# Optimization experiments

Hardware: AMD Instinct MI355X
Metric: run time of the kernel (lower is better)

## Reference

```python
import jax, jax.numpy as jnp
import numpy as np

B, S, D, H = 2, 2048, 768, 12
DK = D // H


def setup_inputs() -> dict:
    key = jax.random.key(0)
    ks = jax.random.split(key, 10)
    sc = 0.02
    return {
        "k": jax.random.normal(ks[0], (B, S, D), jnp.float32),
        "q": jax.random.normal(ks[1], (B, S, D), jnp.float32),
        "v": jax.random.normal(ks[2], (B, S, D), jnp.float32),
        "mask": jnp.ones((B, 1, S, S), jnp.int32),
        "wq": jax.random.normal(ks[3], (D, D), jnp.float32) * sc,
        "bq": jnp.zeros((D,), jnp.float32),
        "wk": jax.random.normal(ks[4], (D, D), jnp.float32) * sc,
        "bk": jnp.zeros((D,), jnp.float32),
        "wv": jax.random.normal(ks[5], (D, D), jnp.float32) * sc,
        "bv": jnp.zeros((D,), jnp.float32),
        "wo": jax.random.normal(ks[6], (D, D), jnp.float32) * sc,
        "bo": jnp.zeros((D,), jnp.float32),
    }


def reference(k, q, v, mask, wq, bq, wk, bk, wv, bv, wo, bo):
    # Linear projections (torch Linear: x @ W^T + b)
    query = q @ wq.T + bq
    key_ = k @ wk.T + bk
    value = v @ wv.T + bv
    # [B,S,D] -> [B,H,S,DK]
    def split_heads(x):
        return x.reshape(B, S, H, DK).transpose(0, 2, 1, 3)
    Q, K, V = split_heads(query), split_heads(key_), split_heads(value)
    # NOTE: original masked_fill result is discarded -> mask is a no-op.
    scores = jnp.einsum("bhqd,bhkd->bhqk", Q, K) / jnp.sqrt(jnp.float32(DK))
    attn = jax.nn.softmax(scores, axis=-1)  # dropout p=0.0 -> identity
    out = jnp.einsum("bhqk,bhkd->bhqd", attn, V)
    out = out.transpose(0, 2, 1, 3).reshape(B, S, D)
    return out @ wo.T + bo
```

## Files before the change

### kernel.cpp

```cpp
#include <hip/hip_runtime.h>
#include <hip/hip_bf16.h>

#define B_  2
#define S_  2048
#define D_  768
#define H_  12
#define DK_ 64
#define NX_ (B_*S_*D_)
#define NW_ (D_*D_)
#define CSC 0.18033688011112042f

typedef __attribute__((ext_vector_type(8))) short  bf16x8;
typedef __attribute__((ext_vector_type(4))) float  f32x4;

__device__ __forceinline__ unsigned short f2bf(float f) {
    unsigned int u = __float_as_uint(f);
    u += 0x7fffu + ((u >> 16) & 1u);
    return (unsigned short)(u >> 16);
}

__device__ __forceinline__ unsigned pack_bf2(float a, float b) {
    const unsigned ua = __float_as_uint(a) + 0x8000u;
    const unsigned ub = __float_as_uint(b) + 0x8000u;
    return __builtin_amdgcn_perm(ub, ua, 0x07060302u);
}

__device__ __forceinline__ void async_cp16(const unsigned short* g,
                                           const unsigned short* lds_uniform_base) {
    __builtin_amdgcn_global_load_lds(
        (const __attribute__((address_space(1))) unsigned int*)(uintptr_t)g,
        (__attribute__((address_space(3))) unsigned int*)(unsigned int)(uintptr_t)lds_uniform_base,
        16, 0, 0);
}

struct CvtArgs { const float* s[7]; };

__global__ __launch_bounds__(256) void cvt_all(CvtArgs a,
                                               unsigned short* __restrict__ Xsw,
                                               unsigned short* __restrict__ Wsw) {
    const int bx = blockIdx.x;
    int y, inner;
    if (bx < 2304) { y = bx / 768;             inner = bx % 768; }
    else           { y = 3 + (bx - 2304) / 144; inner = (bx - 2304) % 144; }
    const int idx = inner * 256 + threadIdx.x;
    const int n  = idx / 48;
    const int g2 = idx % 48;
    const float* src = a.s[y] + (long)n * D_ + g2 * 16;
    const float zs = (y == 3) ? CSC : 1.0f;
    unsigned short o[16];
#pragma unroll
    for (int i = 0; i < 4; i++) {
        const float4 f = *(const float4*)(src + i * 4);
        o[i*4+0] = f2bf(f.x*zs); o[i*4+1] = f2bf(f.y*zs);
        o[i*4+2] = f2bf(f.z*zs); o[i*4+3] = f2bf(f.w*zs);
    }
    unsigned short* dst = (y >= 3) ? (Wsw + (long)(y - 3) * NW_ + (long)n * D_)
                                   : (Xsw + (long)y * NX_ + (long)n * D_);
    const int key = n & 7;
#pragma unroll
    for (int h = 0; h < 2; h++) {
        const int g8 = g2 * 2 + h;
        const int kdst = (g8 >> 3) * 64 + (((g8 & 7) ^ key) * 8);
        *(uint4*)(dst + kdst) = *(const uint4*)&o[h * 8];
    }
}

struct QkvArgs { const float* bias[3]; unsigned short* out[3]; };

__global__ __launch_bounds__(256, 3) void gemm_qkv(QkvArgs args,
                                                   const unsigned short* __restrict__ Xsw,
                                                   const unsigned short* __restrict__ Wsw) {
    __shared__ __align__(16) unsigned short smem[17408];
    unsigned short* As = smem;
    unsigned short* Bs = smem + 8192;

    const int t    = threadIdx.x;
    const int wave = t >> 6;
    const int lane = t & 63;
    const int l16  = lane & 15;
    const int quad = lane >> 4;
    const int wm   = wave >> 1, wn = wave & 1;
    const int m0   = blockIdx.x * 128;
    const int zz   = blockIdx.y / 6;
    const int nb   = blockIdx.y % 6;
    const int n0   = nb * 128;

    const unsigned short* Ap = Xsw + (long)zz * NX_;
    const unsigned short* Wp = Wsw + (long)zz * NW_;

    f32x4 acc[4][4];
#pragma unroll
    for (int s = 0; s < 4; s++)
#pragma unroll
        for (int j = 0; j < 4; j++) acc[s][j] = (f32x4){0.f, 0.f, 0.f, 0.f};

    const int lrow = lane >> 3;
    const int lcg  = lane & 7;

    for (int k0 = 0; k0 < D_; k0 += 64) {
        __syncthreads();
#pragma unroll
        for (int i = 0; i < 4; i++) {
            const int chunk = wave * 4 + i;
            async_cp16(Ap + (long)(m0 + chunk * 8 + lrow) * D_ + k0 + lcg * 8,
                       As + chunk * 512);
        }
#pragma unroll
        for (int i = 0; i < 4; i++) {
            const int chunk = wave * 4 + i;
            async_cp16(Wp + (long)(n0 + chunk * 8 + lrow) * D_ + k0 + lcg * 8,
                       Bs + chunk * 512);
        }
        __syncthreads();
#pragma unroll
        for (int ks = 0; ks < 2; ks++) {
            const int cg = ks * 4 + quad;
            bf16x8 af[4], bf[4];
#pragma unroll
            for (int s = 0; s < 4; s++) {
                const int r = wm * 64 + s * 16 + l16;
                af[s] = *(const bf16x8*)&As[r * 64 + ((cg ^ (r & 7)) * 8)];
            }
#pragma unroll
            for (int j = 0; j < 4; j++) {
                const int r = wn * 64 + j * 16 + l16;
                bf[j] = *(const bf16x8*)&Bs[r * 64 + ((cg ^ (r & 7)) * 8)];
            }
#pragma unroll
            for (int s = 0; s < 4; s++)
#pragma unroll
                for (int j = 0; j < 4; j++)
                    acc[s][j] = __builtin_amdgcn_mfma_f32_16x16x32_bf16(af[s], bf[j], acc[s][j], 0, 0, 0);
        }
    }
    __syncthreads();

    const int b     = m0 >> 11;
    const int sbase = m0 & (S_ - 1);
    const float zs  = (zz == 0) ? CSC : 1.0f;
    float bv[4];
#pragma unroll
    for (int j = 0; j < 4; j++) bv[j] = args.bias[zz][n0 + wn * 64 + j * 16 + l16] * zs;

    if (zz < 2) {
        unsigned short* Ls = smem;
#pragma unroll
        for (int s = 0; s < 4; s++)
#pragma unroll
            for (int j = 0; j < 4; j++)
#pragma unroll
                for (int r = 0; r < 4; r++)
                    Ls[(wm * 64 + s * 16 + quad * 4 + r) * 136 + wn * 64 + j * 16 + l16] =
                        f2bf(acc[s][j][r] + bv[j]);
        __syncthreads();
        const int row  = t >> 1;
        const int half = t & 1;
        unsigned short* Op = args.out[zz];
#pragma unroll
        for (int i = 0; i < 8; i++) {
            const int col  = half * 64 + i * 8;
            const int head = nb * 2 + half;
            const uint4 v = *(const uint4*)&Ls[row * 136 + col];
            *(uint4*)(Op + ((long)(b * H_ + head) * S_ + sbase + row) * DK_ + (col & 63)) = v;
        }
    } else {
        unsigned short* Ls = smem;
#pragma unroll
        for (int s = 0; s < 4; s++)
#pragma unroll
            for (int j = 0; j < 4; j++)
#pragma unroll
                for (int r = 0; r < 4; r++) {
                    const int dk  = j * 16 + l16;
                    const int pos = wm * 64 + (quad * 4 + r) * 4 + s;
                    Ls[wn * 8704 + dk * 136 + pos] = f2bf(acc[s][j][r] + bv[j]);
                }
        __syncthreads();
        const int rowIdx = t >> 1;
        const int hh = rowIdx >> 6, dk = rowIdx & 63;
        const int half = t & 1;
        unsigned short* Op = args.out[2];
#pragma unroll
        for (int i = 0; i < 8; i++) {
            const int col = half * 64 + i * 8;
            const uint4 v = *(const uint4*)&Ls[hh * 8704 + dk * 136 + col];
            const int head = nb * 2 + hh;
            *(uint4*)(Op + ((long)(b * H_ + head) * DK_ + dk) * S_ + sbase + col) = v;
        }
    }
}

__global__ __launch_bounds__(256, 3) void attn_kernel(
    const unsigned short* __restrict__ Q, const unsigned short* __restrict__ K,
    const unsigned short* __restrict__ Vt, unsigned short* __restrict__ Ao)
{
    const int t    = threadIdx.x;
    const int wave = t >> 6;
    const int lane = t & 63;
    const int l16  = lane & 15;
    const int quad = lane >> 4;
    const int bid  = blockIdx.x;
    const int bh    = bid % 24;
    const int qtile = bid / 24;

    const unsigned short* Qp = Q  + (long)bh * S_ * DK_;
    const unsigned short* Kp = K  + (long)bh * S_ * DK_;
    const unsigned short* Vp = Vt + (long)bh * DK_ * S_;

    __shared__ __align__(16) unsigned short smem[23040];
    unsigned short* Ps = smem + 18432;

    bf16x8 qfrag[2];
    {
        const long qoff = (long)(qtile * 64 + wave * 16 + l16) * DK_ + quad * 8;
        qfrag[0] = *(const bf16x8*)(Qp + qoff);
        qfrag[1] = *(const bf16x8*)(Qp + qoff + 32);
    }

    const int srow = t >> 2;
    const int scg  = (t & 3) * 16;
    uint4 kreg[2], vreg[2];
    const unsigned short* gk = Kp + (long)srow * DK_ + scg;
    const unsigned short* gv = Vp + (long)srow * S_ + scg;
    kreg[0] = *(const uint4*)gk;  kreg[1] = *(const uint4*)(gk + 8);
    vreg[0] = *(const uint4*)gv;  vreg[1] = *(const uint4*)(gv + 8);
    gk += 64 * DK_;  gv += 64;
    *(uint4*)&smem[srow * 72 + scg]            = kreg[0];
    *(uint4*)&smem[srow * 72 + scg + 8]        = kreg[1];
    *(uint4*)&smem[9216 + srow * 72 + scg]     = vreg[0];
    *(uint4*)&smem[9216 + srow * 72 + scg + 8] = vreg[1];

    f32x4 oacc[4];
#pragma unroll
    for (int j = 0; j < 4; j++) oacc[j] = (f32x4){0.f, 0.f, 0.f, 0.f};
    float lsum[4] = {0.f, 0.f, 0.f, 0.f};

    for (int it = 0; it < 32; ++it) {
        const int co = (it & 1) * 4608;
        const int no = ((it & 1) ^ 1) * 4608;
        __syncthreads();
        const unsigned short* Ks = smem + co;
        const unsigned short* Vs = smem + 9216 + co;

        if (it < 31) {
            kreg[0] = *(const uint4*)gk;  kreg[1] = *(const uint4*)(gk + 8);
            vreg[0] = *(const uint4*)gv;  vreg[1] = *(const uint4*)(gv + 8);
            gk += 64 * DK_;  gv += 64;
        }

        f32x4 sacc[4];
#pragma unroll
        for (int j = 0; j < 4; j++) sacc[j] = (f32x4){0.f, 0.f, 0.f, 0.f};
#pragma unroll
        for (int ks = 0; ks < 2; ks++)
#pragma unroll
            for (int j = 0; j < 4; j++) {
                const bf16x8 bf = *(const bf16x8*)&Ks[(j * 16 + l16) * 72 + ks * 32 + quad * 8];
                sacc[j] = __builtin_amdgcn_mfma_f32_16x16x32_bf16(qfrag[ks], bf, sacc[j], 0, 0, 0);
            }

#pragma unroll
        for (int r = 0; r < 4; r++) {
            const float p0 = exp2f(sacc[0][r]);
            const float p1 = exp2f(sacc[1][r]);
            const float p2 = exp2f(sacc[2][r]);
            const float p3 = exp2f(sacc[3][r]);
            lsum[r] += (p0 + p1) + (p2 + p3);
            uint2 pk = {pack_bf2(p0, p1), pack_bf2(p2, p3)};
            *(uint2*)&Ps[(wave * 16 + quad * 4 + r) * 72 + l16 * 4] = pk;
        }

#pragma unroll
        for (int ks = 0; ks < 2; ks++) {
            const bf16x8 pf = *(const bf16x8*)&Ps[(wave * 16 + l16) * 72 + ks * 32 + quad * 8];
#pragma unroll
            for (int j = 0; j < 4; j++) {
                const bf16x8 vf = *(const bf16x8*)&Vs[(j * 16 + l16) * 72 + ks * 32 + quad * 8];
                oacc[j] = __builtin_amdgcn_mfma_f32_16x16x32_bf16(pf, vf, oacc[j], 0, 0, 0);
            }
        }

        if (it < 31) {
            *(uint4*)&smem[no + srow * 72 + scg]            = kreg[0];
            *(uint4*)&smem[no + srow * 72 + scg + 8]        = kreg[1];
            *(uint4*)&smem[9216 + no + srow * 72 + scg]     = vreg[0];
            *(uint4*)&smem[9216 + no + srow * 72 + scg + 8] = vreg[1];
        }
    }

#pragma unroll
    for (int r = 0; r < 4; r++) {
#pragma unroll
        for (int off = 1; off < 16; off <<= 1)
            lsum[r] += __shfl_xor(lsum[r], off, 64);
        lsum[r] = 1.f / lsum[r];
    }

    __syncthreads();
#pragma unroll
    for (int j = 0; j < 4; j++)
#pragma unroll
        for (int r = 0; r < 4; r++)
            Ps[(wave * 16 + quad * 4 + r) * 72 + j * 16 + l16] =
                f2bf(oacc[j][r] * lsum[r]);

    const int b = bh / H_, h = bh % H_;
    const int row = t >> 2;
    const int c0  = (t & 3) * 16;
    const int qrow = qtile * 64 + row;
    const int key  = qrow & 7;
    const uint4 v0 = *(const uint4*)&Ps[row * 72 + c0];
    const uint4 v1 = *(const uint4*)&Ps[row * 72 + c0 + 8];
    const int g8 = c0 >> 3;
    unsigned short* dst = Ao + (long)(b * S_ + qrow) * D_ + h * DK_;
    *(uint4*)(dst + ((g8 ^ key) * 8))       = v0;
    *(uint4*)(dst + (((g8 + 1) ^ key) * 8)) = v1;
}

__global__ __launch_bounds__(256, 4) void gemm_out(
    const unsigned short* __restrict__ A, const unsigned short* __restrict__ Wsw,
    const float* __restrict__ bias, float* __restrict__ Out)
{
    __shared__ __align__(16) unsigned short smem[8704];
    unsigned short* As = smem;
    unsigned short* Bs = smem + 4096;

    const int t    = threadIdx.x;
    const int wave = t >> 6;
    const int lane = t & 63;
    const int l16  = lane & 15;
    const int quad = lane >> 4;
    const int wm   = wave >> 1, wn = wave & 1;
    const int m0   = blockIdx.x * 64;
    const int n0   = blockIdx.y * 64;

    f32x4 acc[2][2];
#pragma unroll
    for (int s = 0; s < 2; s++)
#pragma unroll
        for (int j = 0; j < 2; j++) acc[s][j] = (f32x4){0.f, 0.f, 0.f, 0.f};

    const int lrow = lane >> 3;
    const int lcg  = lane & 7;

    for (int k0 = 0; k0 < D_; k0 += 64) {
        __syncthreads();
#pragma unroll
        for (int i = 0; i < 2; i++) {
            const int chunk = wave * 2 + i;
            async_cp16(A + (long)(m0 + chunk * 8 + lrow) * D_ + k0 + lcg * 8,
                       As + chunk * 512);
        }
#pragma unroll
        for (int i = 0; i < 2; i++) {
            const int chunk = wave * 2 + i;
            async_cp16(Wsw + (long)(n0 + chunk * 8 + lrow) * D_ + k0 + lcg * 8,
                       Bs + chunk * 512);
        }
        __syncthreads();
#pragma unroll
        for (int ks = 0; ks < 2; ks++) {
            const int cg = ks * 4 + quad;
            bf16x8 af[2], bf[2];
#pragma unroll
            for (int s = 0; s < 2; s++) {
                const int r = wm * 32 + s * 16 + l16;
                af[s] = *(const bf16x8*)&As[r * 64 + ((cg ^ (r & 7)) * 8)];
            }
#pragma unroll
            for (int j = 0; j < 2; j++) {
                const int r = wn * 32 + j * 16 + l16;
                bf[j] = *(const bf16x8*)&Bs[r * 64 + ((cg ^ (r & 7)) * 8)];
            }
#pragma unroll
            for (int s = 0; s < 2; s++)
#pragma unroll
                for (int j = 0; j < 2; j++)
                    acc[s][j] = __builtin_amdgcn_mfma_f32_16x16x32_bf16(af[s], bf[j], acc[s][j], 0, 0, 0);
        }
    }

    float bv[2];
#pragma unroll
    for (int j = 0; j < 2; j++) bv[j] = bias[n0 + wn * 32 + j * 16 + l16];

    __syncthreads();
    float* fl = (float*)smem;
#pragma unroll
    for (int s = 0; s < 2; s++)
#pragma unroll
        for (int j = 0; j < 2; j++)
#pragma unroll
            for (int r = 0; r < 4; r++)
                fl[(wm * 32 + s * 16 + quad * 4 + r) * 67 + wn * 32 + j * 16 + l16] =
                    acc[s][j][r] + bv[j];
    __syncthreads();
    const int row = t >> 2, c0 = (t & 3) * 16;
#pragma unroll
    for (int i = 0; i < 4; i++) {
        const float4 v = *(const float4*)&fl[row * 67 + c0 + i * 4];
        *(float4*)(Out + (long)(m0 + row) * D_ + n0 + c0 + i * 4) = v;
    }
}

extern "C" void kernel_launch(void* const* d_in, const int* in_sizes, int n_in,
                              void* d_out, int out_size, void* d_ws, size_t ws_size,
                              hipStream_t stream) {
    const float* k_in = (const float*)d_in[0];
    const float* q_in = (const float*)d_in[1];
    const float* v_in = (const float*)d_in[2];
    const float* wq = (const float*)d_in[4];
    const float* bq = (const float*)d_in[5];
    const float* wk = (const float*)d_in[6];
    const float* bk = (const float*)d_in[7];
    const float* wv = (const float*)d_in[8];
    const float* bv = (const float*)d_in[9];
    const float* wo = (const float*)d_in[10];
    const float* bo = (const float*)d_in[11];

    unsigned short* ws = (unsigned short*)d_ws;
    unsigned short* Wsw = ws;
    unsigned short* Qb  = Wsw + 4ll * NW_;
    unsigned short* Kb  = Qb + (long)NX_;
    unsigned short* Vt  = Kb + (long)NX_;
    unsigned short* Xsw = Vt + (long)NX_;
    unsigned short* Ao  = Xsw;

    CvtArgs ca;
    ca.s[0] = q_in; ca.s[1] = k_in; ca.s[2] = v_in;
    ca.s[3] = wq;   ca.s[4] = wk;   ca.s[5] = wv;  ca.s[6] = wo;
    cvt_all<<<dim3(2880), 256, 0, stream>>>(ca, Xsw, Wsw);

    QkvArgs qa;
    qa.bias[0] = bq; qa.bias[1] = bk; qa.bias[2] = bv;
    qa.out[0] = Qb;  qa.out[1] = Kb;  qa.out[2] = Vt;
    gemm_qkv<<<dim3(32, 18), 256, 0, stream>>>(qa, Xsw, Wsw);

    attn_kernel<<<dim3(768), 256, 0, stream>>>(Qb, Kb, Vt, Ao);

    gemm_out<<<dim3(64, 12), 256, 0, stream>>>(Ao, Wsw + 3ll * NW_, bo, (float*)d_out);
}
```

Before: 215.4 us.

## Process 128 query rows per attention block and XOR-swizzle LDS tiles

Each attention block now covers 128 query rows, with each wave handling two 16-row sub-blocks. Every K/V tile staged into shared memory is therefore reused by twice as many queries, halving global K/V traffic and staging work per query. The padded stride-72 LDS layout is replaced by an XOR-swizzled stride-64 layout for K, V, P and the output tile. The output swizzle now matches what gemm_out expects, so the rows can be stored straight from LDS. In exchange, registers per thread roughly double and launch bounds drop to 2 blocks per CU. The grid shrinks to 384 blocks, which may leave some CUs idle or unevenly loaded.

```diff
diff --git a/kernel.cpp b/kernel.cpp
--- a/kernel.cpp
+++ b/kernel.cpp
@@ -190,7 +190,7 @@
     }
 }
 
-__global__ __launch_bounds__(256, 3) void attn_kernel(
+__global__ __launch_bounds__(256, 2) void attn_kernel(
     const unsigned short* __restrict__ Q, const unsigned short* __restrict__ K,
     const unsigned short* __restrict__ Vt, unsigned short* __restrict__ Ao)
 {
@@ -207,40 +207,50 @@
     const unsigned short* Kp = K  + (long)bh * S_ * DK_;
     const unsigned short* Vp = Vt + (long)bh * DK_ * S_;
 
-    __shared__ __align__(16) unsigned short smem[23040];
-    unsigned short* Ps = smem + 18432;
-
-    bf16x8 qfrag[2];
-    {
-        const long qoff = (long)(qtile * 64 + wave * 16 + l16) * DK_ + quad * 8;
-        qfrag[0] = *(const bf16x8*)(Qp + qoff);
-        qfrag[1] = *(const bf16x8*)(Qp + qoff + 32);
+    __shared__ __align__(16) unsigned short smem[24576];
+    unsigned short* Ps = smem + 16384;
+
+    const int fkey = l16 & 7;
+    const int fo0  = (((0 * 4 + quad) ^ fkey) * 8);
+    const int fo1  = (((1 * 4 + quad) ^ fkey) * 8);
+
+    bf16x8 qf[2][2];
+#pragma unroll
+    for (int rb = 0; rb < 2; rb++) {
+        const long qoff = (long)(qtile * 128 + wave * 32 + rb * 16 + l16) * DK_ + quad * 8;
+        qf[rb][0] = *(const bf16x8*)(Qp + qoff);
+        qf[rb][1] = *(const bf16x8*)(Qp + qoff + 32);
     }
 
     const int srow = t >> 2;
-    const int scg  = (t & 3) * 16;
+    const int sc2  = t & 3;
+    const int skey = srow & 7;
+    const int sA   = srow * 64 + (((2 * sc2)     ^ skey) * 8);
+    const int sB   = srow * 64 + (((2 * sc2 + 1) ^ skey) * 8);
     uint4 kreg[2], vreg[2];
-    const unsigned short* gk = Kp + (long)srow * DK_ + scg;
-    const unsigned short* gv = Vp + (long)srow * S_ + scg;
+    const unsigned short* gk = Kp + (long)srow * DK_ + sc2 * 16;
+    const unsigned short* gv = Vp + (long)srow * S_ + sc2 * 16;
     kreg[0] = *(const uint4*)gk;  kreg[1] = *(const uint4*)(gk + 8);
     vreg[0] = *(const uint4*)gv;  vreg[1] = *(const uint4*)(gv + 8);
     gk += 64 * DK_;  gv += 64;
-    *(uint4*)&smem[srow * 72 + scg]            = kreg[0];
-    *(uint4*)&smem[srow * 72 + scg + 8]        = kreg[1];
-    *(uint4*)&smem[9216 + srow * 72 + scg]     = vreg[0];
-    *(uint4*)&smem[9216 + srow * 72 + scg + 8] = vreg[1];
-
-    f32x4 oacc[4];
-#pragma unroll
-    for (int j = 0; j < 4; j++) oacc[j] = (f32x4){0.f, 0.f, 0.f, 0.f};
-    float lsum[4] = {0.f, 0.f, 0.f, 0.f};
+    *(uint4*)&smem[sA]        = kreg[0];
+    *(uint4*)&smem[sB]        = kreg[1];
+    *(uint4*)&smem[8192 + sA] = vreg[0];
+    *(uint4*)&smem[8192 + sB] = vreg[1];
+
+    f32x4 oacc[2][4];
+#pragma unroll
+    for (int rb = 0; rb < 2; rb++)
+#pragma unroll
+        for (int j = 0; j < 4; j++) oacc[rb][j] = (f32x4){0.f, 0.f, 0.f, 0.f};
+    float lsum[2][4] = {{0.f,0.f,0.f,0.f},{0.f,0.f,0.f,0.f}};
 
     for (int it = 0; it < 32; ++it) {
-        const int co = (it & 1) * 4608;
-        const int no = ((it & 1) ^ 1) * 4608;
+        const int co = (it & 1) * 4096;
+        const int no = 4096 - co;
         __syncthreads();
         const unsigned short* Ks = smem + co;
-        const unsigned short* Vs = smem + 9216 + co;
+        const unsigned short* Vs = smem + 8192 + co;
 
         if (it < 31) {
             kreg[0] = *(const uint4*)gk;  kreg[1] = *(const uint4*)(gk + 8);
@@ -248,73 +258,88 @@
             gk += 64 * DK_;  gv += 64;
         }
 
-        f32x4 sacc[4];
-#pragma unroll
-        for (int j = 0; j < 4; j++) sacc[j] = (f32x4){0.f, 0.f, 0.f, 0.f};
-#pragma unroll
-        for (int ks = 0; ks < 2; ks++)
+#pragma unroll
+        for (int rb = 0; rb < 2; rb++) {
+            f32x4 sacc[4];
+#pragma unroll
+            for (int j = 0; j < 4; j++) sacc[j] = (f32x4){0.f, 0.f, 0.f, 0.f};
 #pragma unroll
             for (int j = 0; j < 4; j++) {
-                const bf16x8 bf = *(const bf16x8*)&Ks[(j * 16 + l16) * 72 + ks * 32 + quad * 8];
-                sacc[j] = __builtin_amdgcn_mfma_f32_16x16x32_bf16(qfrag[ks], bf, sacc[j], 0, 0, 0);
-            }
-
+                const bf16x8 bf0 = *(const bf16x8*)&Ks[(j * 16 + l16) * 64 + fo0];
+                sacc[j] = __builtin_amdgcn_mfma_f32_16x16x32_bf16(qf[rb][0], bf0, sacc[j], 0, 0, 0);
+                const bf16x8 bf1 = *(const bf16x8*)&Ks[(j * 16 + l16) * 64 + fo1];
+                sacc[j] = __builtin_amdgcn_mfma_f32_16x16x32_bf16(qf[rb][1], bf1, sacc[j], 0, 0, 0);
+            }
+#pragma unroll
+            for (int r = 0; r < 4; r++) {
+                const float p0 = exp2f(sacc[0][r]);
+                const float p1 = exp2f(sacc[1][r]);
+                const float p2 = exp2f(sacc[2][r]);
+                const float p3 = exp2f(sacc[3][r]);
+                lsum[rb][r] += (p0 + p1) + (p2 + p3);
+                uint2 pk = {pack_bf2(p0, p1), pack_bf2(p2, p3)};
+                const int prow = wave * 32 + rb * 16 + quad * 4 + r;
+                const int padr = prow * 64 + (((l16 >> 1) ^ ((quad * 4 + r) & 7)) * 8)
+                               + (l16 & 1) * 4;
+                *(uint2*)&Ps[padr] = pk;
+            }
+        }
+
+#pragma unroll
+        for (int rb = 0; rb < 2; rb++) {
+#pragma unroll
+            for (int ks = 0; ks < 2; ks++) {
+                const int fo = ks ? fo1 : fo0;
+                const bf16x8 pf = *(const bf16x8*)&Ps[(wave * 32 + rb * 16 + l16) * 64 + fo];
+#pragma unroll
+                for (int j = 0; j < 4; j++) {
+                    const bf16x8 vf = *(const bf16x8*)&Vs[(j * 16 + l16) * 64 + fo];
+                    oacc[rb][j] = __builtin_amdgcn_mfma_f32_16x16x32_bf16(pf, vf, oacc[rb][j], 0, 0, 0);
+                }
+            }
+        }
+
+        if (it < 31) {
+            *(uint4*)&smem[no + sA]        = kreg[0];
+            *(uint4*)&smem[no + sB]        = kreg[1];
+            *(uint4*)&smem[8192 + no + sA] = vreg[0];
+            *(uint4*)&smem[8192 + no + sB] = vreg[1];
+        }
+    }
+
+#pragma unroll
+    for (int rb = 0; rb < 2; rb++)
 #pragma unroll
         for (int r = 0; r < 4; r++) {
-            const float p0 = exp2f(sacc[0][r]);
-            const float p1 = exp2f(sacc[1][r]);
-            const float p2 = exp2f(sacc[2][r]);
-            const float p3 = exp2f(sacc[3][r]);
-            lsum[r] += (p0 + p1) + (p2 + p3);
-            uint2 pk = {pack_bf2(p0, p1), pack_bf2(p2, p3)};
-            *(uint2*)&Ps[(wave * 16 + quad * 4 + r) * 72 + l16 * 4] = pk;
-        }
-
-#pragma unroll
-        for (int ks = 0; ks < 2; ks++) {
-            const bf16x8 pf = *(const bf16x8*)&Ps[(wave * 16 + l16) * 72 + ks * 32 + quad * 8];
-#pragma unroll
-            for (int j = 0; j < 4; j++) {
-                const bf16x8 vf = *(const bf16x8*)&Vs[(j * 16 + l16) * 72 + ks * 32 + quad * 8];
-                oacc[j] = __builtin_amdgcn_mfma_f32_16x16x32_bf16(pf, vf, oacc[j], 0, 0, 0);
-            }
-        }
-
-        if (it < 31) {
-            *(uint4*)&smem[no + srow * 72 + scg]            = kreg[0];
-            *(uint4*)&smem[no + srow * 72 + scg + 8]        = kreg[1];
-            *(uint4*)&smem[9216 + no + srow * 72 + scg]     = vreg[0];
-            *(uint4*)&smem[9216 + no + srow * 72 + scg + 8] = vreg[1];
-        }
-    }
-
-#pragma unroll
-    for (int r = 0; r < 4; r++) {
-#pragma unroll
-        for (int off = 1; off < 16; off <<= 1)
-            lsum[r] += __shfl_xor(lsum[r], off, 64);
-        lsum[r] = 1.f / lsum[r];
-    }
+#pragma unroll
+            for (int off = 1; off < 16; off <<= 1)
+                lsum[rb][r] += __shfl_xor(lsum[rb][r], off, 64);
+            lsum[rb][r] = 1.f / lsum[rb][r];
+        }
 
     __syncthreads();
 #pragma unroll
-    for (int j = 0; j < 4; j++)
-#pragma unroll
-        for (int r = 0; r < 4; r++)
-            Ps[(wave * 16 + quad * 4 + r) * 72 + j * 16 + l16] =
-                f2bf(oacc[j][r] * lsum[r]);
-
+    for (int rb = 0; rb < 2; rb++)
+#pragma unroll
+        for (int j = 0; j < 4; j++)
+#pragma unroll
+            for (int r = 0; r < 4; r++) {
+                const int row = wave * 32 + rb * 16 + quad * 4 + r;
+                const int key = (quad * 4 + r) & 7;
+                const int c   = j * 2 + (l16 >> 3);
+                Ps[row * 64 + ((c ^ key) * 8) + (l16 & 7)] =
+                    f2bf(oacc[rb][j][r] * lsum[rb][r]);
+            }
+
+    const int row  = t >> 1;
+    const int qrow = qtile * 128 + row;
     const int b = bh / H_, h = bh % H_;
-    const int row = t >> 2;
-    const int c0  = (t & 3) * 16;
-    const int qrow = qtile * 64 + row;
-    const int key  = qrow & 7;
-    const uint4 v0 = *(const uint4*)&Ps[row * 72 + c0];
-    const uint4 v1 = *(const uint4*)&Ps[row * 72 + c0 + 8];
-    const int g8 = c0 >> 3;
     unsigned short* dst = Ao + (long)(b * S_ + qrow) * D_ + h * DK_;
-    *(uint4*)(dst + ((g8 ^ key) * 8))       = v0;
-    *(uint4*)(dst + (((g8 + 1) ^ key) * 8)) = v1;
+#pragma unroll
+    for (int i = 0; i < 4; i++) {
+        const int p = (t & 1) * 4 + i;
+        *(uint4*)(dst + p * 8) = *(const uint4*)&Ps[row * 64 + p * 8];
+    }
 }
 
 __global__ __launch_bounds__(256, 4) void gemm_out(
@@ -436,7 +461,7 @@
     qa.out[0] = Qb;  qa.out[1] = Kb;  qa.out[2] = Vt;
     gemm_qkv<<<dim3(32, 18), 256, 0, stream>>>(qa, Xsw, Wsw);
 
-    attn_kernel<<<dim3(768), 256, 0, stream>>>(Qb, Kb, Vt, Ao);
+    attn_kernel<<<dim3(384), 256, 0, stream>>>(Qb, Kb, Vt, Ao);
 
     gemm_out<<<dim3(64, 12), 256, 0, stream>>>(Ao, Wsw + 3ll * NW_, bo, (float*)d_out);
 }
```

New measurement: 225.8 us. 4.9% more time.
